# Performance work log

Hardware: AMD Instinct MI355X
Metric: run time of the kernel (lower is better)

The kernel has to match this reference:

```python
import jax, jax.numpy as jnp
import numpy as np

B, S, RNN, ATTH = 256, 196, 1024, 512  # batch, att_size, rnn_size, att_h_size


def setup_inputs() -> dict:
    key = jax.random.key(0)
    k1, k2, k3, k4, k5, k6, k7 = jax.random.split(key, 7)
    h = jax.random.normal(k1, (B, RNN), dtype=jnp.float32)
    att_feats = jax.random.normal(k2, (B, S, RNN), dtype=jnp.float32)
    p_att_feats = jax.random.normal(k3, (B, S, ATTH), dtype=jnp.float32)
    # learned params (torch nn.Linear: y = x @ W.T + b)
    w_h2att = jax.random.normal(k4, (ATTH, RNN), dtype=jnp.float32) / np.sqrt(RNN)
    b_h2att = jax.random.normal(k5, (ATTH,), dtype=jnp.float32) * 0.01
    w_alpha = jax.random.normal(k6, (1, ATTH), dtype=jnp.float32) / np.sqrt(ATTH)
    b_alpha = jax.random.normal(k7, (1,), dtype=jnp.float32) * 0.01
    return {
        "h": h,
        "att_feats": att_feats,
        "p_att_feats": p_att_feats,
        "w_h2att": w_h2att,
        "b_h2att": b_h2att,
        "w_alpha": w_alpha,
        "b_alpha": b_alpha,
    }


def reference(h, att_feats, p_att_feats, w_h2att, b_h2att, w_alpha, b_alpha):
    # att_h = h2att(h): [B, ATTH]
    att_h = h @ w_h2att.T + b_h2att
    # additive combine + tanh: [B, S, ATTH]
    dot = jnp.tanh(p_att_feats + att_h[:, None, :])
    # alpha_net: [B, S]
    scores = jnp.einsum("bsa,a->bs", dot, w_alpha[0]) + b_alpha[0]
    weight = jax.nn.softmax(scores, axis=1)
    # weighted sum of att_feats: [B, RNN]
    att_res = jnp.einsum("bs,bsd->bd", weight, att_feats)
    return att_res
```

## Files before the change

kernel.cpp:

```cpp
#include <hip/hip_runtime.h>
#include <cstddef>

static constexpr int kB    = 256;
static constexpr int kS    = 196;
static constexpr int kRNN  = 1024;
static constexpr int kATTH = 512;

__device__ __forceinline__ float fast_tanh(float x) {
    x = fminf(12.0f, fmaxf(-12.0f, x));
    float e = __expf(2.0f * x);
    return __fdividef(e - 1.0f, e + 1.0f);
}

__global__ __launch_bounds__(256) void gemm_atth(
    const float* __restrict__ h, const float* __restrict__ w,
    const float* __restrict__ bias, float* __restrict__ att_h) {
    __shared__ float As[32][33];
    __shared__ float Bs[32][33];
    const int bm = blockIdx.x * 32;
    const int bn = blockIdx.y * 32;
    const int tid = threadIdx.x;
    const int lrow = tid >> 3;
    const int lcol = (tid & 7) << 2;
    const int tx = tid & 31;
    const int ty = tid >> 5;
    float acc[4] = {0.f, 0.f, 0.f, 0.f};
    for (int k0 = 0; k0 < kRNN; k0 += 32) {
        float4 av = *(const float4*)&h[(size_t)(bm + lrow) * kRNN + k0 + lcol];
        float4 bv = *(const float4*)&w[(size_t)(bn + lrow) * kRNN + k0 + lcol];
        As[lrow][lcol + 0] = av.x; As[lrow][lcol + 1] = av.y;
        As[lrow][lcol + 2] = av.z; As[lrow][lcol + 3] = av.w;
        Bs[lrow][lcol + 0] = bv.x; Bs[lrow][lcol + 1] = bv.y;
        Bs[lrow][lcol + 2] = bv.z; Bs[lrow][lcol + 3] = bv.w;
        __syncthreads();
#pragma unroll
        for (int k = 0; k < 32; ++k) {
            float bb = Bs[tx][k];
#pragma unroll
            for (int i = 0; i < 4; ++i) acc[i] += As[ty * 4 + i][k] * bb;
        }
        __syncthreads();
    }
    const float bval = bias[bn + tx];
#pragma unroll
    for (int i = 0; i < 4; ++i)
        att_h[(size_t)(bm + ty * 4 + i) * kATTH + bn + tx] = acc[i] + bval;
}

__global__ __launch_bounds__(1024) void att_fused(
    const float* __restrict__ att_feats, const float* __restrict__ p_att,
    const float* __restrict__ att_h, const float* __restrict__ w_alpha,
    const float* __restrict__ b_alpha, float* __restrict__ out) {
    const int b = blockIdx.x;
    const int tid = threadIdx.x;
    const int lane = tid & 63;
    const int wave = tid >> 6;

    __shared__ float sScore[kS];
    __shared__ float4 sRed[3][256];

    const int col = lane << 3;
    const float4 ah0 = *(const float4*)&att_h[(size_t)b * kATTH + col];
    const float4 ah1 = *(const float4*)&att_h[(size_t)b * kATTH + col + 4];
    const float4 wa0 = *(const float4*)&w_alpha[col];
    const float4 wa1 = *(const float4*)&w_alpha[col + 4];
    const float balpha = b_alpha[0];

    for (int s = wave; s < kS; s += 16) {
        const float* p = &p_att[((size_t)b * kS + s) * kATTH + col];
        const float4 p0 = *(const float4*)p;
        const float4 p1 = *(const float4*)(p + 4);
        float partial;
        partial  = fast_tanh(p0.x + ah0.x) * wa0.x;
        partial += fast_tanh(p0.y + ah0.y) * wa0.y;
        partial += fast_tanh(p0.z + ah0.z) * wa0.z;
        partial += fast_tanh(p0.w + ah0.w) * wa0.w;
        partial += fast_tanh(p1.x + ah1.x) * wa1.x;
        partial += fast_tanh(p1.y + ah1.y) * wa1.y;
        partial += fast_tanh(p1.z + ah1.z) * wa1.z;
        partial += fast_tanh(p1.w + ah1.w) * wa1.w;
#pragma unroll
        for (int off = 32; off > 0; off >>= 1)
            partial += __shfl_xor(partial, off, 64);
        if (lane == 0) sScore[s] = partial + balpha;
    }
    __syncthreads();

    if (tid < 64) {
        float vals[4];
        int cnt = 0;
        float m = -3.0e38f;
        for (int s = tid; s < kS; s += 64) {
            vals[cnt] = sScore[s];
            m = fmaxf(m, vals[cnt]);
            ++cnt;
        }
#pragma unroll
        for (int off = 32; off > 0; off >>= 1) m = fmaxf(m, __shfl_xor(m, off, 64));
        float sum = 0.f;
        for (int i = 0; i < cnt; ++i) { vals[i] = __expf(vals[i] - m); sum += vals[i]; }
#pragma unroll
        for (int off = 32; off > 0; off >>= 1) sum += __shfl_xor(sum, off, 64);
        const float inv = __fdividef(1.0f, sum);
        cnt = 0;
        for (int s = tid; s < kS; s += 64) { sScore[s] = vals[cnt] * inv; ++cnt; }
    }
    __syncthreads();

    const int d4 = tid & 255;
    const int sg = tid >> 8;
    float4 acc = {0.f, 0.f, 0.f, 0.f};
    for (int s = sg; s < kS; s += 4) {
        const float ws = sScore[s];
        const float4 v =
            *(const float4*)&att_feats[((size_t)b * kS + s) * kRNN + (d4 << 2)];
        acc.x += ws * v.x; acc.y += ws * v.y;
        acc.z += ws * v.z; acc.w += ws * v.w;
    }
    if (sg > 0) sRed[sg - 1][d4] = acc;
    __syncthreads();
    if (sg == 0) {
        const float4 r0 = sRed[0][d4];
        const float4 r1 = sRed[1][d4];
        const float4 r2 = sRed[2][d4];
        acc.x += r0.x + r1.x + r2.x;
        acc.y += r0.y + r1.y + r2.y;
        acc.z += r0.z + r1.z + r2.z;
        acc.w += r0.w + r1.w + r2.w;
        *(float4*)&out[(size_t)b * kRNN + (d4 << 2)] = acc;
    }
}

extern "C" void kernel_launch(void* const* d_in, const int* in_sizes, int n_in,
                              void* d_out, int out_size, void* d_ws, size_t ws_size,
                              hipStream_t stream) {
    const float* h         = (const float*)d_in[0];
    const float* att_feats = (const float*)d_in[1];
    const float* p_att     = (const float*)d_in[2];
    const float* w_h2att   = (const float*)d_in[3];
    const float* b_h2att   = (const float*)d_in[4];
    const float* w_alpha   = (const float*)d_in[5];
    const float* b_alpha   = (const float*)d_in[6];
    float* out = (float*)d_out;
    float* att_h = (float*)d_ws;

    dim3 g1(kB / 32, kATTH / 32);
    gemm_atth<<<g1, 256, 0, stream>>>(h, w_h2att, b_h2att, att_h);
    att_fused<<<kB, 1024, 0, stream>>>(att_feats, p_att, att_h, w_alpha, b_alpha, out);
}
```

Baseline: 427.4 us.

## Fuse h2att GEMV into attention kernel and unroll score and weighted-sum loops

Removes the separate tiled GEMM launch: each block computes its own att_h row as a GEMV over w_h2att, with one wave reduction per output, and keeps the result in shared memory. The score loop now handles two sequence positions per iteration, and the weighted-sum loop gets a fixed trip count with unrolling, so more loads are in flight. The aim is to drop one launch and the att_h round trip through global memory. The cost is that every block re-reads the full 2MB w_h2att matrix (served from L2), which adds serial work before the memory-bound phase.

```diff
diff --git a/kernel.cpp b/kernel.cpp
--- a/kernel.cpp
+++ b/kernel.cpp
@@ -12,77 +12,97 @@
     return __fdividef(e - 1.0f, e + 1.0f);
 }
 
-__global__ __launch_bounds__(256) void gemm_atth(
-    const float* __restrict__ h, const float* __restrict__ w,
-    const float* __restrict__ bias, float* __restrict__ att_h) {
-    __shared__ float As[32][33];
-    __shared__ float Bs[32][33];
-    const int bm = blockIdx.x * 32;
-    const int bn = blockIdx.y * 32;
-    const int tid = threadIdx.x;
-    const int lrow = tid >> 3;
-    const int lcol = (tid & 7) << 2;
-    const int tx = tid & 31;
-    const int ty = tid >> 5;
-    float acc[4] = {0.f, 0.f, 0.f, 0.f};
-    for (int k0 = 0; k0 < kRNN; k0 += 32) {
-        float4 av = *(const float4*)&h[(size_t)(bm + lrow) * kRNN + k0 + lcol];
-        float4 bv = *(const float4*)&w[(size_t)(bn + lrow) * kRNN + k0 + lcol];
-        As[lrow][lcol + 0] = av.x; As[lrow][lcol + 1] = av.y;
-        As[lrow][lcol + 2] = av.z; As[lrow][lcol + 3] = av.w;
-        Bs[lrow][lcol + 0] = bv.x; Bs[lrow][lcol + 1] = bv.y;
-        Bs[lrow][lcol + 2] = bv.z; Bs[lrow][lcol + 3] = bv.w;
-        __syncthreads();
-#pragma unroll
-        for (int k = 0; k < 32; ++k) {
-            float bb = Bs[tx][k];
-#pragma unroll
-            for (int i = 0; i < 4; ++i) acc[i] += As[ty * 4 + i][k] * bb;
-        }
-        __syncthreads();
-    }
-    const float bval = bias[bn + tx];
-#pragma unroll
-    for (int i = 0; i < 4; ++i)
-        att_h[(size_t)(bm + ty * 4 + i) * kATTH + bn + tx] = acc[i] + bval;
+__device__ __forceinline__ float dot8t(const float4 p0, const float4 p1,
+                                       const float4 ah0, const float4 ah1,
+                                       const float4 wa0, const float4 wa1) {
+    float r;
+    r  = fast_tanh(p0.x + ah0.x) * wa0.x;
+    r += fast_tanh(p0.y + ah0.y) * wa0.y;
+    r += fast_tanh(p0.z + ah0.z) * wa0.z;
+    r += fast_tanh(p0.w + ah0.w) * wa0.w;
+    r += fast_tanh(p1.x + ah1.x) * wa1.x;
+    r += fast_tanh(p1.y + ah1.y) * wa1.y;
+    r += fast_tanh(p1.z + ah1.z) * wa1.z;
+    r += fast_tanh(p1.w + ah1.w) * wa1.w;
+    return r;
 }
 
-__global__ __launch_bounds__(1024) void att_fused(
-    const float* __restrict__ att_feats, const float* __restrict__ p_att,
-    const float* __restrict__ att_h, const float* __restrict__ w_alpha,
-    const float* __restrict__ b_alpha, float* __restrict__ out) {
+__global__ __launch_bounds__(1024) void att_one(
+    const float* __restrict__ h,
+    const float* __restrict__ att_feats,
+    const float* __restrict__ p_att,
+    const float* __restrict__ w_h2att,
+    const float* __restrict__ b_h2att,
+    const float* __restrict__ w_alpha,
+    const float* __restrict__ b_alpha,
+    float* __restrict__ out) {
     const int b = blockIdx.x;
     const int tid = threadIdx.x;
     const int lane = tid & 63;
     const int wave = tid >> 6;
 
+    __shared__ float sAttH[kATTH];
     __shared__ float sScore[kS];
     __shared__ float4 sRed[3][256];
 
-    const int col = lane << 3;
-    const float4 ah0 = *(const float4*)&att_h[(size_t)b * kATTH + col];
-    const float4 ah1 = *(const float4*)&att_h[(size_t)b * kATTH + col + 4];
-    const float4 wa0 = *(const float4*)&w_alpha[col];
-    const float4 wa1 = *(const float4*)&w_alpha[col + 4];
-    const float balpha = b_alpha[0];
+    {
+        const float* hb = &h[(size_t)b * kRNN];
+        const int k0 = lane << 2;
+        const float4 h0 = *(const float4*)&hb[k0];
+        const float4 h1 = *(const float4*)&hb[k0 + 256];
+        const float4 h2 = *(const float4*)&hb[k0 + 512];
+        const float4 h3 = *(const float4*)&hb[k0 + 768];
+        const int abase = wave << 5;
+#pragma unroll 2
+        for (int r = 0; r < 32; ++r) {
+            const int a = abase + r;
+            const float* wr = &w_h2att[(size_t)a * kRNN + k0];
+            const float4 x0 = *(const float4*)(wr);
+            const float4 x1 = *(const float4*)(wr + 256);
+            const float4 x2 = *(const float4*)(wr + 512);
+            const float4 x3 = *(const float4*)(wr + 768);
+            float d;
+            d  = x0.x * h0.x + x0.y * h0.y + x0.z * h0.z + x0.w * h0.w;
+            d += x1.x * h1.x + x1.y * h1.y + x1.z * h1.z + x1.w * h1.w;
+            d += x2.x * h2.x + x2.y * h2.y + x2.z * h2.z + x2.w * h2.w;
+            d += x3.x * h3.x + x3.y * h3.y + x3.z * h3.z + x3.w * h3.w;
+#pragma unroll
+            for (int off = 32; off > 0; off >>= 1) d += __shfl_xor(d, off, 64);
+            if (lane == 0) sAttH[a] = d + b_h2att[a];
+        }
+    }
+    __syncthreads();
 
-    for (int s = wave; s < kS; s += 16) {
-        const float* p = &p_att[((size_t)b * kS + s) * kATTH + col];
-        const float4 p0 = *(const float4*)p;
-        const float4 p1 = *(const float4*)(p + 4);
-        float partial;
-        partial  = fast_tanh(p0.x + ah0.x) * wa0.x;
-        partial += fast_tanh(p0.y + ah0.y) * wa0.y;
-        partial += fast_tanh(p0.z + ah0.z) * wa0.z;
-        partial += fast_tanh(p0.w + ah0.w) * wa0.w;
-        partial += fast_tanh(p1.x + ah1.x) * wa1.x;
-        partial += fast_tanh(p1.y + ah1.y) * wa1.y;
-        partial += fast_tanh(p1.z + ah1.z) * wa1.z;
-        partial += fast_tanh(p1.w + ah1.w) * wa1.w;
+    {
+        const int col = lane << 3;
+        const float4 ah0 = *(const float4*)&sAttH[col];
+        const float4 ah1 = *(const float4*)&sAttH[col + 4];
+        const float4 wa0 = *(const float4*)&w_alpha[col];
+        const float4 wa1 = *(const float4*)&w_alpha[col + 4];
+        const float balpha = b_alpha[0];
+
+        for (int s = wave; s < kS; s += 32) {
+            const int s2 = s + 16;
+            const float* p = &p_att[((size_t)b * kS + s) * kATTH + col];
+            const float4 p0 = *(const float4*)p;
+            const float4 p1 = *(const float4*)(p + 4);
+            float4 q0 = {0.f, 0.f, 0.f, 0.f}, q1 = {0.f, 0.f, 0.f, 0.f};
+            if (s2 < kS) {
+                const float* q = p + (size_t)16 * kATTH;
+                q0 = *(const float4*)q;
+                q1 = *(const float4*)(q + 4);
+            }
+            float r1 = dot8t(p0, p1, ah0, ah1, wa0, wa1);
 #pragma unroll
-        for (int off = 32; off > 0; off >>= 1)
-            partial += __shfl_xor(partial, off, 64);
-        if (lane == 0) sScore[s] = partial + balpha;
+            for (int off = 32; off > 0; off >>= 1) r1 += __shfl_xor(r1, off, 64);
+            if (lane == 0) sScore[s] = r1 + balpha;
+            if (s2 < kS) {
+                float r2 = dot8t(q0, q1, ah0, ah1, wa0, wa1);
+#pragma unroll
+                for (int off = 32; off > 0; off >>= 1) r2 += __shfl_xor(r2, off, 64);
+                if (lane == 0) sScore[s2] = r2 + balpha;
+            }
+        }
     }
     __syncthreads();
 
@@ -109,11 +129,13 @@
 
     const int d4 = tid & 255;
     const int sg = tid >> 8;
+    const float* af = &att_feats[(size_t)b * kS * kRNN + (d4 << 2)];
     float4 acc = {0.f, 0.f, 0.f, 0.f};
-    for (int s = sg; s < kS; s += 4) {
+#pragma unroll 4
+    for (int i = 0; i < 49; ++i) {
+        const int s = (i << 2) + sg;
         const float ws = sScore[s];
-        const float4 v =
-            *(const float4*)&att_feats[((size_t)b * kS + s) * kRNN + (d4 << 2)];
+        const float4 v = *(const float4*)&af[(size_t)s * kRNN];
         acc.x += ws * v.x; acc.y += ws * v.y;
         acc.z += ws * v.z; acc.w += ws * v.w;
     }
@@ -142,9 +164,7 @@
     const float* w_alpha   = (const float*)d_in[5];
     const float* b_alpha   = (const float*)d_in[6];
     float* out = (float*)d_out;
-    float* att_h = (float*)d_ws;
 
-    dim3 g1(kB / 32, kATTH / 32);
-    gemm_atth<<<g1, 256, 0, stream>>>(h, w_h2att, b_h2att, att_h);
-    att_fused<<<kB, 1024, 0, stream>>>(att_feats, p_att, att_h, w_alpha, b_alpha, out);
+    att_one<<<kB, 1024, 0, stream>>>(h, att_feats, p_att, w_h2att, b_h2att,
+                                     w_alpha, b_alpha, out);
 }
```

New measurement: 383.8 us. 1.11x faster.
